# Optimization experiments

Measured on AMD Instinct MI355X. Metric: run time of the kernel, lower is better.

## Reference

```python
import jax, jax.numpy as jnp
import numpy as np


def setup_inputs() -> dict:
    key = jax.random.key(0)
    k1, k2, k3, k4 = jax.random.split(key, 4)
    B, L, R, H, D = 64, 512, 512, 512, 256
    return {
        "lstm_lt": jax.random.normal(k1, (B, L, H), dtype=jnp.float32),
        "lstm_rt": jax.random.normal(k2, (B, R, H), dtype=jnp.float32),
        "atten_W": jax.random.normal(k3, (H, D), dtype=jnp.float32) * 0.05,
        "diagnoal_W": jax.random.normal(k4, (1, 1, D), dtype=jnp.float32) * 0.05,
    }


def reference(lstm_lt, lstm_rt, atten_W, diagnoal_W):
    # Projection (the original's broadcast-multiply-sum is exactly a GEMM):
    # atten_lt[b,l,d] = tanh(sum_h lstm_lt[b,l,h] * W[h,d]) * diag_W[d]
    atten_lt = jnp.tanh(jnp.einsum('blh,hd->bld', lstm_lt, atten_W)) * diagnoal_W
    atten_rt = jnp.tanh(jnp.einsum('brh,hd->brd', lstm_rt, atten_W))
    # batch_dot over the attention dim -> (B, L, R)
    atten_value = jnp.einsum('bld,brd->blr', atten_lt, atten_rt)
    # No masks supplied (len(inputs)==2 path); softmax over last axis.
    return jax.nn.softmax(atten_value, axis=-1)
```

## Files before the change

### kernel.cpp

```cpp
#include <hip/hip_runtime.h>

typedef __attribute__((ext_vector_type(8))) __bf16 bf16x8;
typedef __attribute__((ext_vector_type(4))) float f32x4;

#define DI __device__ __forceinline__

DI unsigned short f2bf(float x) {
  unsigned u = __float_as_uint(x);
  u += 0x7fffu + ((u >> 16) & 1u);
  return (unsigned short)(u >> 16);
}

DI bf16x8 cvt8(f32x4 lo, f32x4 hi) {
  bf16x8 r;
  r[0] = (__bf16)lo.x; r[1] = (__bf16)lo.y; r[2] = (__bf16)lo.z; r[3] = (__bf16)lo.w;
  r[4] = (__bf16)hi.x; r[5] = (__bf16)hi.y; r[6] = (__bf16)hi.z; r[7] = (__bf16)hi.w;
  return r;
}

DI float tanh_fast(float x) {
  float ax = fabsf(x);
  float e = __expf(-2.0f * ax);
  float t = (1.0f - e) / (1.0f + e);
  return x < 0.0f ? -t : t;
}

DI void glds16(const void* gptr, void* lptr) {
  __builtin_amdgcn_global_load_lds(
      (const __attribute__((address_space(1))) unsigned int*)gptr,
      (__attribute__((address_space(3))) unsigned int*)lptr, 16, 0, 0);
}

__global__ void k_wt(const float* __restrict__ W, unsigned short* __restrict__ Wt) {
  int n = blockIdx.x;
  int t = threadIdx.x;
  int k = t * 4;
  ushort4 v;
  v.x = f2bf(W[(k + 0) * 256 + n]);
  v.y = f2bf(W[(k + 1) * 256 + n]);
  v.z = f2bf(W[(k + 2) * 256 + n]);
  v.w = f2bf(W[(k + 3) * 256 + n]);
  *(ushort4*)&Wt[n * 512 + k] = v;
}

__global__ __launch_bounds__(512, 4) void k_proj(
    const float* __restrict__ Alt, const float* __restrict__ Art,
    const unsigned short* __restrict__ Wt, const float* __restrict__ diag,
    unsigned short* __restrict__ Olt, unsigned short* __restrict__ Ort) {
  __shared__ __align__(16) float As[128 * 64];
  __shared__ __align__(16) unsigned short Bs[256 * 64];

  int bx = blockIdx.x;
  bool is_lt = bx < 256;
  int m0 = (is_lt ? bx : bx - 256) * 128;
  const char* Abase = (const char*)((is_lt ? Alt : Art) + (size_t)m0 * 512);
  unsigned short* O = (is_lt ? Olt : Ort) + (size_t)m0 * 256;

  int tid  = threadIdx.x;
  int lane = tid & 63;
  int wid  = tid >> 6;
  int wm   = wid >> 2;
  int wn   = wid & 3;
  int l15  = lane & 15;
  int quad = lane >> 4;
  int r7   = l15 & 7;

  int lr4 = lane >> 4, c16 = lane & 15;
  int aoff = lr4 * 2048 + ((c16 ^ lr4) << 4);
  int lr8 = lane >> 3, s8 = lane & 7;
  int boff = lr8 * 1024 + ((s8 ^ lr8) << 4);

  const char* Bbase = (const char*)Wt;
  char* AsB = (char*)As;
  char* BsB = (char*)Bs;

  f32x4 zero = {0.0f, 0.0f, 0.0f, 0.0f};
  f32x4 acc[4][4];
#pragma unroll
  for (int i = 0; i < 4; i++)
#pragma unroll
    for (int j = 0; j < 4; j++) acc[i][j] = zero;

  for (int k0 = 0; k0 < 512; k0 += 64) {
#pragma unroll
    for (int i = 0; i < 4; i++) {
      int j = wid * 4 + i;
      glds16(Abase + (size_t)j * 8192 + (size_t)k0 * 4 + (aoff ^ ((j & 1) << 6)),
             AsB + j * 1024);
    }
#pragma unroll
    for (int i = 0; i < 4; i++) {
      int j = wid * 4 + i;
      glds16(Bbase + (size_t)j * 8192 + (size_t)k0 * 2 + boff, BsB + j * 1024);
    }
    __syncthreads();

#pragma unroll
    for (int ks = 0; ks < 2; ks++) {
      bf16x8 a[4], b[4];
#pragma unroll
      for (int mt = 0; mt < 4; mt++) {
        int row = wm * 64 + mt * 16 + l15;
        int c0 = ks * 8 + quad * 2;
        f32x4 lo = *(const f32x4*)(AsB + row * 256 + (((c0    ) ^ r7) << 4));
        f32x4 hi = *(const f32x4*)(AsB + row * 256 + (((c0 + 1) ^ r7) << 4));
        a[mt] = cvt8(lo, hi);
      }
#pragma unroll
      for (int nt = 0; nt < 4; nt++) {
        int row = wn * 64 + nt * 16 + l15;
        int c = ks * 4 + quad;
        b[nt] = *(const bf16x8*)(BsB + row * 128 + ((c ^ r7) << 4));
      }
#pragma unroll
      for (int mt = 0; mt < 4; mt++)
#pragma unroll
        for (int nt = 0; nt < 4; nt++)
          acc[mt][nt] = __builtin_amdgcn_mfma_f32_16x16x32_bf16(a[mt], b[nt], acc[mt][nt], 0, 0, 0);
    }
    __syncthreads();
  }

  float dscale[4];
#pragma unroll
  for (int nt = 0; nt < 4; nt++)
    dscale[nt] = is_lt ? diag[wn * 64 + nt * 16 + l15] : 1.0f;

#pragma unroll
  for (int mt = 0; mt < 4; mt++) {
#pragma unroll
    for (int r = 0; r < 4; r++) {
      int row = wm * 64 + mt * 16 + quad * 4 + r;
#pragma unroll
      for (int nt = 0; nt < 4; nt++) {
        int col = wn * 64 + nt * 16 + l15;
        O[(size_t)row * 256 + col] = f2bf(tanh_fast(acc[mt][nt][r]) * dscale[nt]);
      }
    }
  }
}

__global__ __launch_bounds__(512, 4) void k_attn(
    const unsigned short* __restrict__ Lt, const unsigned short* __restrict__ Rt,
    float* __restrict__ Out) {
  __shared__ __align__(16) unsigned short Ls[64 * 64];
  __shared__ __align__(16) unsigned short Rs[512 * 64];
  __shared__ float red[8][64];
  __shared__ float rowv[64];

  int bx = blockIdx.x;
  int b  = (bx & 7) * 8 + ((bx >> 3) & 7);
  int l0 = (bx >> 6) * 64;
  const char* Lb = (const char*)(Lt + ((size_t)b * 512 + l0) * 256);
  const char* Rb = (const char*)(Rt + (size_t)b * 512 * 256);
  float* Ob = Out + ((size_t)b * 512 + l0) * 512;

  int tid  = threadIdx.x;
  int lane = tid & 63;
  int wid  = tid >> 6;
  int l15  = lane & 15;
  int quad = lane >> 4;
  int r7   = l15 & 7;

  int lr8 = lane >> 3, s8 = lane & 7;
  int goff = lr8 * 512 + ((s8 ^ lr8) << 4);

  char* LsB = (char*)Ls;
  char* RsB = (char*)Rs;

  f32x4 zero = {0.0f, 0.0f, 0.0f, 0.0f};
  f32x4 acc[4][4];
#pragma unroll
  for (int i = 0; i < 4; i++)
#pragma unroll
    for (int j = 0; j < 4; j++) acc[i][j] = zero;

  for (int k0 = 0; k0 < 256; k0 += 64) {
    glds16(Lb + (size_t)wid * 4096 + (size_t)k0 * 2 + goff, LsB + wid * 1024);
#pragma unroll
    for (int i = 0; i < 8; i++) {
      int j = wid * 8 + i;
      glds16(Rb + (size_t)j * 4096 + (size_t)k0 * 2 + goff, RsB + j * 1024);
    }
    __syncthreads();

#pragma unroll
    for (int ks = 0; ks < 2; ks++) {
      bf16x8 a[4], bb[4];
#pragma unroll
      for (int mt = 0; mt < 4; mt++) {
        int row = mt * 16 + l15;
        int c = ks * 4 + quad;
        a[mt] = *(const bf16x8*)(LsB + row * 128 + ((c ^ r7) << 4));
      }
#pragma unroll
      for (int nt = 0; nt < 4; nt++) {
        int row = wid * 64 + nt * 16 + l15;
        int c = ks * 4 + quad;
        bb[nt] = *(const bf16x8*)(RsB + row * 128 + ((c ^ r7) << 4));
      }
#pragma unroll
      for (int mt = 0; mt < 4; mt++)
#pragma unroll
        for (int nt = 0; nt < 4; nt++)
          acc[mt][nt] = __builtin_amdgcn_mfma_f32_16x16x32_bf16(a[mt], bb[nt], acc[mt][nt], 0, 0, 0);
    }
    __syncthreads();
  }

#pragma unroll
  for (int mt = 0; mt < 4; mt++) {
#pragma unroll
    for (int r = 0; r < 4; r++) {
      float m = fmaxf(fmaxf(acc[mt][0][r], acc[mt][1][r]),
                      fmaxf(acc[mt][2][r], acc[mt][3][r]));
      m = fmaxf(m, __shfl_xor(m, 1));
      m = fmaxf(m, __shfl_xor(m, 2));
      m = fmaxf(m, __shfl_xor(m, 4));
      m = fmaxf(m, __shfl_xor(m, 8));
      if (l15 == 0) red[wid][mt * 16 + quad * 4 + r] = m;
    }
  }
  __syncthreads();
  if (tid < 64) {
    float m = red[0][tid];
#pragma unroll
    for (int w = 1; w < 8; w++) m = fmaxf(m, red[w][tid]);
    rowv[tid] = m;
  }
  __syncthreads();

#pragma unroll
  for (int mt = 0; mt < 4; mt++) {
#pragma unroll
    for (int r = 0; r < 4; r++) {
      float base = rowv[mt * 16 + quad * 4 + r];
      float s = 0.0f;
#pragma unroll
      for (int nt = 0; nt < 4; nt++) {
        float e = __expf(acc[mt][nt][r] - base);
        acc[mt][nt][r] = e;
        s += e;
      }
      s += __shfl_xor(s, 1);
      s += __shfl_xor(s, 2);
      s += __shfl_xor(s, 4);
      s += __shfl_xor(s, 8);
      if (l15 == 0) red[wid][mt * 16 + quad * 4 + r] = s;
    }
  }
  __syncthreads();
  if (tid < 64) {
    float s = red[0][tid];
#pragma unroll
    for (int w = 1; w < 8; w++) s += red[w][tid];
    rowv[tid] = 1.0f / s;
  }
  __syncthreads();

#pragma unroll
  for (int mt = 0; mt < 4; mt++) {
#pragma unroll
    for (int r = 0; r < 4; r++) {
      int row = mt * 16 + quad * 4 + r;
      float inv = rowv[row];
#pragma unroll
      for (int nt = 0; nt < 4; nt++) {
        int col = wid * 64 + nt * 16 + l15;
        Ob[(size_t)row * 512 + col] = acc[mt][nt][r] * inv;
      }
    }
  }
}

extern "C" void kernel_launch(void* const* d_in, const int* in_sizes, int n_in,
                              void* d_out, int out_size, void* d_ws, size_t ws_size,
                              hipStream_t stream) {
  const float* lstm_lt = (const float*)d_in[0];
  const float* lstm_rt = (const float*)d_in[1];
  const float* W       = (const float*)d_in[2];
  const float* diag    = (const float*)d_in[3];
  float* out = (float*)d_out;

  unsigned short* Wt  = (unsigned short*)d_ws;
  unsigned short* Olt = (unsigned short*)((char*)d_ws + (size_t)256 * 512 * 2);
  unsigned short* Ort = Olt + (size_t)32768 * 256;

  k_wt<<<dim3(256), dim3(128), 0, stream>>>(W, Wt);
  k_proj<<<dim3(512), dim3(512), 0, stream>>>(lstm_lt, lstm_rt, Wt, diag, Olt, Ort);
  k_attn<<<dim3(512), dim3(512), 0, stream>>>(Olt, Ort, out);
}
```

Baseline: 208.0 us.

## Load unshared GEMM operands directly from global into registers, double-buffer weights

```diff
diff --git a/kernel.cpp b/kernel.cpp
--- a/kernel.cpp
+++ b/kernel.cpp
@@ -47,93 +47,95 @@
     const float* __restrict__ Alt, const float* __restrict__ Art,
     const unsigned short* __restrict__ Wt, const float* __restrict__ diag,
     unsigned short* __restrict__ Olt, unsigned short* __restrict__ Ort) {
-  __shared__ __align__(16) float As[128 * 64];
-  __shared__ __align__(16) unsigned short Bs[256 * 64];
+  __shared__ __align__(16) unsigned short Bs[2][256 * 64];
 
   int bx = blockIdx.x;
   bool is_lt = bx < 256;
   int m0 = (is_lt ? bx : bx - 256) * 128;
-  const char* Abase = (const char*)((is_lt ? Alt : Art) + (size_t)m0 * 512);
+  const float* A = (is_lt ? Alt : Art) + (size_t)m0 * 512;
   unsigned short* O = (is_lt ? Olt : Ort) + (size_t)m0 * 256;
 
   int tid  = threadIdx.x;
   int lane = tid & 63;
   int wid  = tid >> 6;
-  int wm   = wid >> 2;
-  int wn   = wid & 3;
+  int wm   = wid >> 1;
+  int wn   = wid & 1;
   int l15  = lane & 15;
   int quad = lane >> 4;
-  int r7   = l15 & 7;
-
-  int lr4 = lane >> 4, c16 = lane & 15;
-  int aoff = lr4 * 2048 + ((c16 ^ lr4) << 4);
-  int lr8 = lane >> 3, s8 = lane & 7;
-  int boff = lr8 * 1024 + ((s8 ^ lr8) << 4);
-
-  const char* Bbase = (const char*)Wt;
-  char* AsB = (char*)As;
-  char* BsB = (char*)Bs;
+  int lr8  = lane >> 3;
+  int s8   = lane & 7;
+
+  const char* Wb = (const char*)Wt;
+  int bsrc = lr8 * 1024 + ((s8 ^ lr8) << 4);
+
+  const float* ap0 = A + (size_t)(wm * 32 + 0 * 16 + l15) * 512 + quad * 8;
+  const float* ap1 = A + (size_t)(wm * 32 + 1 * 16 + l15) * 512 + quad * 8;
 
   f32x4 zero = {0.0f, 0.0f, 0.0f, 0.0f};
-  f32x4 acc[4][4];
-#pragma unroll
-  for (int i = 0; i < 4; i++)
-#pragma unroll
-    for (int j = 0; j < 4; j++) acc[i][j] = zero;
-
-  for (int k0 = 0; k0 < 512; k0 += 64) {
-#pragma unroll
-    for (int i = 0; i < 4; i++) {
-      int j = wid * 4 + i;
-      glds16(Abase + (size_t)j * 8192 + (size_t)k0 * 4 + (aoff ^ ((j & 1) << 6)),
-             AsB + j * 1024);
-    }
-#pragma unroll
-    for (int i = 0; i < 4; i++) {
-      int j = wid * 4 + i;
-      glds16(Bbase + (size_t)j * 8192 + (size_t)k0 * 2 + boff, BsB + j * 1024);
+  f32x4 acc[2][8];
+#pragma unroll
+  for (int i = 0; i < 2; i++)
+#pragma unroll
+    for (int j = 0; j < 8; j++) acc[i][j] = zero;
+
+#pragma unroll
+  for (int i = 0; i < 4; i++) {
+    int j = wid * 4 + i;
+    glds16(Wb + (size_t)j * 8192 + bsrc, (char*)Bs[0] + j * 1024);
+  }
+  __syncthreads();
+
+  for (int kw = 0; kw < 8; kw++) {
+    int cur = kw & 1;
+    if (kw < 7) {
+#pragma unroll
+      for (int i = 0; i < 4; i++) {
+        int j = wid * 4 + i;
+        glds16(Wb + (size_t)j * 8192 + (kw + 1) * 128 + bsrc,
+               (char*)Bs[cur ^ 1] + j * 1024);
+      }
+    }
+    const char* Bc = (const char*)Bs[cur];
+#pragma unroll
+    for (int ks = 0; ks < 2; ks++) {
+      bf16x8 a[2], b[8];
+      {
+        f32x4 lo0 = *(const f32x4*)(ap0 + kw * 64 + ks * 32);
+        f32x4 hi0 = *(const f32x4*)(ap0 + kw * 64 + ks * 32 + 4);
+        f32x4 lo1 = *(const f32x4*)(ap1 + kw * 64 + ks * 32);
+        f32x4 hi1 = *(const f32x4*)(ap1 + kw * 64 + ks * 32 + 4);
+        a[0] = cvt8(lo0, hi0);
+        a[1] = cvt8(lo1, hi1);
+      }
+#pragma unroll
+      for (int nt = 0; nt < 8; nt++) {
+        int n = wn * 128 + nt * 16 + l15;
+        int c = ks * 4 + quad;
+        b[nt] = *(const bf16x8*)(Bc + (n >> 3) * 1024 + (n & 7) * 128 +
+                                 ((c ^ (n & 7)) << 4));
+      }
+#pragma unroll
+      for (int mt = 0; mt < 2; mt++)
+#pragma unroll
+        for (int nt = 0; nt < 8; nt++)
+          acc[mt][nt] = __builtin_amdgcn_mfma_f32_16x16x32_bf16(a[mt], b[nt], acc[mt][nt], 0, 0, 0);
     }
     __syncthreads();
-
-#pragma unroll
-    for (int ks = 0; ks < 2; ks++) {
-      bf16x8 a[4], b[4];
-#pragma unroll
-      for (int mt = 0; mt < 4; mt++) {
-        int row = wm * 64 + mt * 16 + l15;
-        int c0 = ks * 8 + quad * 2;
-        f32x4 lo = *(const f32x4*)(AsB + row * 256 + (((c0    ) ^ r7) << 4));
-        f32x4 hi = *(const f32x4*)(AsB + row * 256 + (((c0 + 1) ^ r7) << 4));
-        a[mt] = cvt8(lo, hi);
-      }
-#pragma unroll
-      for (int nt = 0; nt < 4; nt++) {
-        int row = wn * 64 + nt * 16 + l15;
-        int c = ks * 4 + quad;
-        b[nt] = *(const bf16x8*)(BsB + row * 128 + ((c ^ r7) << 4));
-      }
-#pragma unroll
-      for (int mt = 0; mt < 4; mt++)
-#pragma unroll
-        for (int nt = 0; nt < 4; nt++)
-          acc[mt][nt] = __builtin_amdgcn_mfma_f32_16x16x32_bf16(a[mt], b[nt], acc[mt][nt], 0, 0, 0);
-    }
-    __syncthreads();
-  }
-
-  float dscale[4];
-#pragma unroll
-  for (int nt = 0; nt < 4; nt++)
-    dscale[nt] = is_lt ? diag[wn * 64 + nt * 16 + l15] : 1.0f;
-
-#pragma unroll
-  for (int mt = 0; mt < 4; mt++) {
-#pragma unroll
-    for (int r = 0; r < 4; r++) {
-      int row = wm * 64 + mt * 16 + quad * 4 + r;
-#pragma unroll
-      for (int nt = 0; nt < 4; nt++) {
-        int col = wn * 64 + nt * 16 + l15;
+  }
+
+  float dscale[8];
+#pragma unroll
+  for (int nt = 0; nt < 8; nt++)
+    dscale[nt] = is_lt ? diag[wn * 128 + nt * 16 + l15] : 1.0f;
+
+#pragma unroll
+  for (int mt = 0; mt < 2; mt++) {
+#pragma unroll
+    for (int r = 0; r < 4; r++) {
+      int row = wm * 32 + mt * 16 + quad * 4 + r;
+#pragma unroll
+      for (int nt = 0; nt < 8; nt++) {
+        int col = wn * 128 + nt * 16 + l15;
         O[(size_t)row * 256 + col] = f2bf(tanh_fast(acc[mt][nt][r]) * dscale[nt]);
       }
     }
@@ -143,8 +145,7 @@
 __global__ __launch_bounds__(512, 4) void k_attn(
     const unsigned short* __restrict__ Lt, const unsigned short* __restrict__ Rt,
     float* __restrict__ Out) {
-  __shared__ __align__(16) unsigned short Ls[64 * 64];
-  __shared__ __align__(16) unsigned short Rs[512 * 64];
+  __shared__ __align__(16) unsigned short Ls[64 * 256];
   __shared__ float red[8][64];
   __shared__ float rowv[64];
 
@@ -152,7 +153,7 @@
   int b  = (bx & 7) * 8 + ((bx >> 3) & 7);
   int l0 = (bx >> 6) * 64;
   const char* Lb = (const char*)(Lt + ((size_t)b * 512 + l0) * 256);
-  const char* Rb = (const char*)(Rt + (size_t)b * 512 * 256);
+  const unsigned short* Rb = Rt + (size_t)b * 512 * 256;
   float* Ob = Out + ((size_t)b * 512 + l0) * 512;
 
   int tid  = threadIdx.x;
@@ -160,13 +161,22 @@
   int wid  = tid >> 6;
   int l15  = lane & 15;
   int quad = lane >> 4;
-  int r7   = l15 & 7;
-
-  int lr8 = lane >> 3, s8 = lane & 7;
-  int goff = lr8 * 512 + ((s8 ^ lr8) << 4);
-
-  char* LsB = (char*)Ls;
-  char* RsB = (char*)Rs;
+  int lr8  = lane >> 3;
+  int s8   = lane & 7;
+
+#pragma unroll
+  for (int i = 0; i < 4; i++) {
+    int j = wid * 4 + i;
+    int rg = j >> 2, rq = j & 3;
+    glds16(Lb + (size_t)(rg * 8 + lr8) * 512 + rq * 128 + ((s8 ^ lr8) << 4),
+           (char*)Ls + j * 1024);
+  }
+  __syncthreads();
+
+  const unsigned short* bp[4];
+#pragma unroll
+  for (int nt = 0; nt < 4; nt++)
+    bp[nt] = Rb + (size_t)(wid * 64 + nt * 16 + l15) * 256 + quad * 8;
 
   f32x4 zero = {0.0f, 0.0f, 0.0f, 0.0f};
   f32x4 acc[4][4];
@@ -175,37 +185,24 @@
 #pragma unroll
     for (int j = 0; j < 4; j++) acc[i][j] = zero;
 
-  for (int k0 = 0; k0 < 256; k0 += 64) {
-    glds16(Lb + (size_t)wid * 4096 + (size_t)k0 * 2 + goff, LsB + wid * 1024);
-#pragma unroll
-    for (int i = 0; i < 8; i++) {
-      int j = wid * 8 + i;
-      glds16(Rb + (size_t)j * 4096 + (size_t)k0 * 2 + goff, RsB + j * 1024);
-    }
-    __syncthreads();
-
-#pragma unroll
-    for (int ks = 0; ks < 2; ks++) {
-      bf16x8 a[4], bb[4];
-#pragma unroll
-      for (int mt = 0; mt < 4; mt++) {
-        int row = mt * 16 + l15;
-        int c = ks * 4 + quad;
-        a[mt] = *(const bf16x8*)(LsB + row * 128 + ((c ^ r7) << 4));
-      }
-#pragma unroll
-      for (int nt = 0; nt < 4; nt++) {
-        int row = wid * 64 + nt * 16 + l15;
-        int c = ks * 4 + quad;
-        bb[nt] = *(const bf16x8*)(RsB + row * 128 + ((c ^ r7) << 4));
-      }
-#pragma unroll
-      for (int mt = 0; mt < 4; mt++)
-#pragma unroll
-        for (int nt = 0; nt < 4; nt++)
-          acc[mt][nt] = __builtin_amdgcn_mfma_f32_16x16x32_bf16(a[mt], bb[nt], acc[mt][nt], 0, 0, 0);
-    }
-    __syncthreads();
+#pragma unroll
+  for (int ks = 0; ks < 8; ks++) {
+    bf16x8 a[4], bb[4];
+#pragma unroll
+    for (int nt = 0; nt < 4; nt++)
+      bb[nt] = *(const bf16x8*)(bp[nt] + ks * 32);
+#pragma unroll
+    for (int mt = 0; mt < 4; mt++) {
+      int r = mt * 16 + l15;
+      int c = ks * 4 + quad;
+      a[mt] = *(const bf16x8*)((const char*)Ls + (r >> 3) * 4096 + (c >> 3) * 1024 +
+                               (r & 7) * 128 + (((c & 7) ^ (r & 7)) << 4));
+    }
+#pragma unroll
+    for (int mt = 0; mt < 4; mt++)
+#pragma unroll
+      for (int nt = 0; nt < 4; nt++)
+        acc[mt][nt] = __builtin_amdgcn_mfma_f32_16x16x32_bf16(a[mt], bb[nt], acc[mt][nt], 0, 0, 0);
   }
 
 #pragma unroll
```

Result: slower. 223.7 us (+7.5%).
